# Performance work log

Hardware: AMD Instinct MI355X
Metric: run time of the kernel (lower is better)

## Reference

```python
import jax, jax.numpy as jnp
import numpy as np

B, S = 4, 2048
DM, H, DK, DV, DI = 512, 4, 128, 128, 1024
NT, NV = 64, 5000
PAD = 0


def layernorm(x, g, b, eps=1e-5):
    m = jnp.mean(x, axis=-1, keepdims=True)
    v = jnp.var(x, axis=-1, keepdims=True)
    return (x - m) * jax.lax.rsqrt(v + eps) * g + b


def setup_inputs() -> dict:
    key = jax.random.key(0)
    ks = jax.random.split(key, 20)
    event_type = jax.random.randint(ks[0], (B, S), 0, NT + 1)
    vertex = jax.random.randint(ks[1], (B, S), 0, NV + 1)
    vertex = jnp.where(event_type == PAD, 0, vertex)  # align padding
    event_time = jnp.sort(jax.random.uniform(ks[2], (B, S)) * 100.0, axis=1)
    non_pad_mask = (event_type != PAD).astype(jnp.float32)[..., None]  # [B,S,1]
    sc = 0.02
    event_emb = jax.random.normal(ks[3], (NT + 1, DM)) * sc
    event_emb = event_emb.at[PAD].set(0.0)
    vertex_emb = jax.random.normal(ks[4], (NV + 1, DM)) * sc
    vertex_emb = vertex_emb.at[PAD].set(0.0)
    A = jax.random.uniform(ks[5], (NV, NV))
    W = jax.random.uniform(ks[6], (NV, NV))
    Wq = jax.random.normal(ks[7], (DM, H * DK)) * sc
    Wk = jax.random.normal(ks[8], (DM, H * DK)) * sc
    Wv = jax.random.normal(ks[9], (DM, H * DV)) * sc
    Wo = jax.random.normal(ks[10], (H * DV, DM)) * sc
    bo = jnp.zeros((DM,))
    ln1_g, ln1_b = jnp.ones((DM,)), jnp.zeros((DM,))
    w1 = jax.random.normal(ks[11], (DM, DI)) * sc
    b1 = jnp.zeros((DI,))
    w2 = jax.random.normal(ks[12], (DI, DM)) * sc
    b2 = jnp.zeros((DM,))
    ln2_g, ln2_b = jnp.ones((DM,)), jnp.zeros((DM,))
    return dict(event_type=event_type, vertex=vertex, event_time=event_time,
                non_pad_mask=non_pad_mask, A=A, W=W, event_emb=event_emb,
                vertex_emb=vertex_emb, Wq=Wq, Wk=Wk, Wv=Wv, Wo=Wo, bo=bo,
                ln1_g=ln1_g, ln1_b=ln1_b, w1=w1, b1=b1, w2=w2, b2=b2,
                ln2_g=ln2_g, ln2_b=ln2_b)


def similarity(vertex, A, W):
    # vectorized form of the triple-loop pairwise gather: [B,1,S,S]
    idx = jnp.clip(vertex - 1, 0)                       # [B,S]
    vm = (vertex != 0)
    pair = vm[:, :, None] & vm[:, None, :]              # [B,S,S]
    sim = A[idx[:, :, None], idx[:, None, :]] * W[idx[:, :, None], idx[:, None, :]] * 10.0
    return (sim * pair.astype(A.dtype))[:, None]        # [B,1,S,S]


def temporal_enc(event_time, non_pad_mask, d_model):
    i = jnp.arange(d_model)
    pv = jnp.power(jnp.float32(10000.0), 2.0 * (i // 2).astype(jnp.float32) / d_model)
    r = event_time[:, :, None] / pv                     # [B,S,D]
    return jnp.where(i % 2 == 0, jnp.sin(r), jnp.cos(r)) * non_pad_mask


def reference(event_type, vertex, event_time, non_pad_mask, A, W, event_emb,
              vertex_emb, Wq, Wk, Wv, Wo, bo, ln1_g, ln1_b, w1, b1, w2, b2,
              ln2_g, ln2_b):
    b_, s_ = event_type.shape
    # masks: key-padding OR subsequent (causal)
    pad = (event_type == PAD)
    subseq = jnp.triu(jnp.ones((s_, s_), dtype=bool), 1)
    slf_attn_mask = pad[:, None, :] | subseq[None]      # [B,S,S]

    sim = similarity(vertex, A, W)                      # [B,1,S,S]
    tem = temporal_enc(event_time, non_pad_mask, DM)    # [B,S,D]
    ver = vertex_emb[vertex]                            # [B,S,D]
    enc = event_emb[event_type]                         # [B,S,D]

    # single encoder layer (n_layers=1), post-norm THP-style
    enc = enc + ver + tem
    res = enc
    q = (enc @ Wq).reshape(b_, s_, H, DK)
    k = (enc @ Wk).reshape(b_, s_, H, DK)
    v = (enc @ Wv).reshape(b_, s_, H, DV)
    scores = jnp.einsum('bihd,bjhd->bhij', q, k) / jnp.sqrt(jnp.float32(DK)) + sim
    scores = jnp.where(slf_attn_mask[:, None], jnp.float32(-1e9), scores)
    attn = jax.nn.softmax(scores, axis=-1)
    o = jnp.einsum('bhij,bjhd->bihd', attn, v).reshape(b_, s_, H * DV)
    o = o @ Wo + bo
    enc = layernorm(o + res, ln1_g, ln1_b) * non_pad_mask
    res = enc
    f = jax.nn.relu(enc @ w1 + b1) @ w2 + b2
    enc = layernorm(f + res, ln2_g, ln2_b) * non_pad_mask
    return enc, sim
```

## Files before the change

### kernel.cpp

```cpp
#include <hip/hip_runtime.h>
#include <hip/hip_bf16.h>

#define B_ 4
#define S_ 2048
#define DM_ 512
#define H_ 4
#define DK_ 128
#define DI_ 1024
#define NV_ 5000

typedef __attribute__((ext_vector_type(8))) short bf16x8;
typedef __attribute__((ext_vector_type(8))) unsigned short u16x8;
typedef __attribute__((ext_vector_type(4))) unsigned short u16x4;
typedef __attribute__((ext_vector_type(4))) float f32x4;

__device__ inline unsigned short f2bf(float x) {
  unsigned int u = __float_as_uint(x);
  unsigned int r = (u + 0x7fffu + ((u >> 16) & 1u)) >> 16;
  return (unsigned short)r;
}
__device__ inline float bf2f(unsigned short u) {
  return __uint_as_float(((unsigned int)u) << 16);
}
__device__ inline void gload16(const void* g, void* l) {
  __builtin_amdgcn_global_load_lds(
      (const __attribute__((address_space(1))) void*)g,
      (__attribute__((address_space(3))) void*)l, 16, 0, 0);
}

__global__ __launch_bounds__(256) void embed_kernel(
    const int* __restrict__ et, const int* __restrict__ vx,
    const float* __restrict__ tmv, const float* __restrict__ npm,
    const float* __restrict__ eemb, const float* __restrict__ vemb,
    float* __restrict__ enc0, unsigned short* __restrict__ enc0b) {
  int row = blockIdx.x;
  int t = et[row], v = vx[row];
  float time = tmv[row], mask = npm[row];
  int tid = threadIdx.x;
  #pragma unroll
  for (int k = 0; k < 2; ++k) {
    int dd = tid + k * 256;
    float pvinv = __expf((float)(dd & ~1) * -0.017988946039015984f);
    float r = time * pvinv;
    float tem = (((dd & 1) == 0) ? sinf(r) : cosf(r)) * mask;
    float val = eemb[(size_t)t * DM_ + dd] + vemb[(size_t)v * DM_ + dd] + tem;
    enc0[(size_t)row * DM_ + dd] = val;
    enc0b[(size_t)row * DM_ + dd] = f2bf(val);
  }
}

__global__ __launch_bounds__(256) void sim_kernel(
    const int* __restrict__ vx, const float* __restrict__ A,
    const float* __restrict__ W, float* __restrict__ sim) {
  __shared__ __attribute__((aligned(16))) float Ar[5120];
  __shared__ __attribute__((aligned(16))) float Wr[5120];
  int i = blockIdx.x;
  int b = blockIdx.y;
  int vi = vx[b * S_ + i];
  float* out = sim + ((size_t)(b * S_ + i)) * S_;
  int tid = threadIdx.x;
  if (vi == 0) {
    for (int j = tid * 4; j < S_; j += 1024)
      *(float4*)&out[j] = (float4){0.f, 0.f, 0.f, 0.f};
    return;
  }
  int w = tid >> 6, l = tid & 63;
  const char* Abase = (const char*)(A + (size_t)(vi - 1) * NV_);
  const char* Wbase = (const char*)(W + (size_t)(vi - 1) * NV_);
  #pragma unroll
  for (int it = 0; it < 5; ++it) {
    int seg = it * 4 + w;
    int chunk = seg * 64 + l;
    if (chunk < 1250) {
      gload16(Abase + (size_t)chunk * 16, (char*)Ar + seg * 1024);
      gload16(Wbase + (size_t)chunk * 16, (char*)Wr + seg * 1024);
    }
  }
  asm volatile("s_waitcnt vmcnt(0)" ::: "memory");
  __syncthreads();
  for (int j = tid * 4; j < S_; j += 1024) {
    int4 vj = *(const int4*)&vx[b * S_ + j];
    float4 o;
    o.x = vj.x ? Ar[vj.x - 1] * Wr[vj.x - 1] * 10.0f : 0.f;
    o.y = vj.y ? Ar[vj.y - 1] * Wr[vj.y - 1] * 10.0f : 0.f;
    o.z = vj.z ? Ar[vj.z - 1] * Wr[vj.z - 1] * 10.0f : 0.f;
    o.w = vj.w ? Ar[vj.w - 1] * Wr[vj.w - 1] * 10.0f : 0.f;
    *(float4*)&out[j] = o;
  }
}

__global__ __launch_bounds__(256) void wt_all_kernel(
    const float* __restrict__ Wq, const float* __restrict__ Wk,
    const float* __restrict__ Wv, const float* __restrict__ Wo,
    const float* __restrict__ w1, const float* __restrict__ w2,
    unsigned short* __restrict__ WqT, unsigned short* __restrict__ WkT,
    unsigned short* __restrict__ WvT, unsigned short* __restrict__ WoT,
    unsigned short* __restrict__ w1T, unsigned short* __restrict__ w2T) {
  __shared__ unsigned short T[32][40];
  int bid = blockIdx.x;
  const float* src; unsigned short* dst; int K, N, lid;
  if (bid < 256)       { src = Wq; dst = WqT; K = 512;  N = 512;  lid = bid; }
  else if (bid < 512)  { src = Wk; dst = WkT; K = 512;  N = 512;  lid = bid - 256; }
  else if (bid < 768)  { src = Wv; dst = WvT; K = 512;  N = 512;  lid = bid - 512; }
  else if (bid < 1024) { src = Wo; dst = WoT; K = 512;  N = 512;  lid = bid - 768; }
  else if (bid < 1536) { src = w1; dst = w1T; K = 512;  N = 1024; lid = bid - 1024; }
  else                 { src = w2; dst = w2T; K = 1024; N = 512;  lid = bid - 1536; }
  int nt = N / 32;
  int n0 = (lid % nt) * 32, k0 = (lid / nt) * 32;
  int r = threadIdx.x >> 3, c0 = (threadIdx.x & 7) * 4;
  float4 v = *(const float4*)&src[(size_t)(k0 + r) * N + n0 + c0];
  T[r][c0 + 0] = f2bf(v.x);
  T[r][c0 + 1] = f2bf(v.y);
  T[r][c0 + 2] = f2bf(v.z);
  T[r][c0 + 3] = f2bf(v.w);
  __syncthreads();
  u16x4 o;
  o[0] = T[c0 + 0][r]; o[1] = T[c0 + 1][r];
  o[2] = T[c0 + 2][r]; o[3] = T[c0 + 3][r];
  *(u16x4*)&dst[(size_t)(n0 + r) * K + k0 + c0] = o;
}

template <int OMODE, bool RELU, int MT = 128>
__global__ __launch_bounds__(256) void gemm_bf16_kernel(
    const unsigned short* __restrict__ A, const unsigned short* __restrict__ BT,
    const float* __restrict__ bias, void* __restrict__ C,
    int M, int N, int K) {
  __shared__ __attribute__((aligned(16))) unsigned short As[MT][72];
  __shared__ __attribute__((aligned(16))) unsigned short Bs[128][72];
  int tid = threadIdx.x;
  int w = tid >> 6, l = tid & 63;
  int l16 = l & 15, lh = l >> 4;
  const int NFR = (MT == 128) ? 4 : 2;
  int wr = (MT == 128) ? (w >> 1) : 0;
  int wc = (MT == 128) ? (w & 1) : w;
  int row0 = blockIdx.y * MT, col0 = blockIdx.x * 128;
  int ra = tid >> 1, ha = (tid & 1) * 32;
  f32x4 acc[4][4];
  #pragma unroll
  for (int m = 0; m < 4; ++m)
    #pragma unroll
    for (int n = 0; n < NFR; ++n) acc[m][n] = (f32x4){0.f, 0.f, 0.f, 0.f};

  for (int k0 = 0; k0 < K; k0 += 64) {
    __syncthreads();
    if (MT == 128) {
      const unsigned short* sa = &A[(size_t)(row0 + ra) * K + k0 + ha];
      uint4 a0 = *(const uint4*)(sa);
      uint4 a1 = *(const uint4*)(sa + 8);
      uint4 a2 = *(const uint4*)(sa + 16);
      uint4 a3 = *(const uint4*)(sa + 24);
      *(uint4*)&As[ra][ha + 0] = a0;
      *(uint4*)&As[ra][ha + 8] = a1;
      *(uint4*)&As[ra][ha + 16] = a2;
      *(uint4*)&As[ra][ha + 24] = a3;
    } else {
      int ra2 = tid >> 2, ha2 = (tid & 3) * 16;
      const unsigned short* sa = &A[(size_t)(row0 + ra2) * K + k0 + ha2];
      uint4 a0 = *(const uint4*)(sa);
      uint4 a1 = *(const uint4*)(sa + 8);
      *(uint4*)&As[ra2][ha2 + 0] = a0;
      *(uint4*)&As[ra2][ha2 + 8] = a1;
    }
    {
      const unsigned short* sb = &BT[(size_t)(col0 + ra) * K + k0 + ha];
      uint4 b0 = *(const uint4*)(sb);
      uint4 b1 = *(const uint4*)(sb + 8);
      uint4 b2 = *(const uint4*)(sb + 16);
      uint4 b3 = *(const uint4*)(sb + 24);
      *(uint4*)&Bs[ra][ha + 0] = b0;
      *(uint4*)&Bs[ra][ha + 8] = b1;
      *(uint4*)&Bs[ra][ha + 16] = b2;
      *(uint4*)&Bs[ra][ha + 24] = b3;
    }
    __syncthreads();
    #pragma unroll
    for (int kc = 0; kc < 2; ++kc) {
      bf16x8 af[4], bfr[4];
      #pragma unroll
      for (int m = 0; m < 4; ++m)
        af[m] = *(bf16x8*)&As[wr * 64 + m * 16 + l16][kc * 32 + lh * 8];
      #pragma unroll
      for (int n = 0; n < NFR; ++n)
        bfr[n] = *(bf16x8*)&Bs[wc * (16 * NFR) + n * 16 + l16][kc * 32 + lh * 8];
      #pragma unroll
      for (int m = 0; m < 4; ++m)
        #pragma unroll
        for (int n = 0; n < NFR; ++n)
          acc[m][n] = __builtin_amdgcn_mfma_f32_16x16x32_bf16(af[m], bfr[n], acc[m][n], 0, 0, 0);
    }
  }
  #pragma unroll
  for (int m = 0; m < 4; ++m) {
    #pragma unroll
    for (int r = 0; r < 4; ++r) {
      int row = row0 + wr * 64 + m * 16 + lh * 4 + r;
      #pragma unroll
      for (int n = 0; n < NFR; ++n) {
        int colg = col0 + wc * (16 * NFR) + n * 16 + l16;
        float v = acc[m][n][r];
        if (bias) v += bias[colg];
        if (RELU) v = fmaxf(v, 0.f);
        if (OMODE == 0) {
          ((float*)C)[(size_t)row * N + colg] = v;
        } else if (OMODE == 1) {
          ((unsigned short*)C)[(size_t)row * N + colg] = f2bf(v);
        } else {
          int which = colg >> 9;
          int cl = colg & 511;
          int b = row >> 11, s = row & 2047;
          int h = cl >> 7, d = cl & 127;
          unsigned short* base =
              (unsigned short*)C + (size_t)which * (4194304);
          if (which < 2)
            base[((size_t)((b * 4 + h) * 2048 + s)) * 128 + d] = f2bf(v);
          else
            base[((size_t)((b * 4 + h) * 128 + d)) * 2048 + s] = f2bf(v);
        }
      }
    }
  }
}

__global__ __launch_bounds__(256) void attn_mfma_kernel(
    const unsigned short* __restrict__ Qb, const unsigned short* __restrict__ Kb,
    const unsigned short* __restrict__ Vt, const float* __restrict__ sim,
    const float* __restrict__ npm, unsigned short* __restrict__ Op0,
    unsigned short* __restrict__ Op1, float2* __restrict__ ml0,
    float2* __restrict__ ml1) {
  __shared__ __attribute__((aligned(16))) char KsL[2][16384];
  __shared__ __attribute__((aligned(16))) char VtsL[2][16384];
  __shared__ __attribute__((aligned(16))) unsigned short Pl[4][16][72];
  int bid = blockIdx.x;
  int xcd = bid & 7;
  int j0 = bid >> 3;
  int bh = xcd * 2 + (j0 & 1);
  int jj = j0 >> 1;
  int pair = jj & 15;
  int half = jj >> 4;
  int b = bh >> 2;
  int tid = threadIdx.x;
  int w = tid >> 6, l = tid & 63;
  int l16 = l & 15, lh = l >> 4;
  unsigned short* Op = half ? Op1 : Op0;
  float2* ml = half ? ml1 : ml0;

  const char* KbB = (const char*)Kb + (size_t)bh * 2048 * 256;
  const char* VtB = (const char*)Vt + (size_t)bh * 128 * 4096;
  int krow[4], kcol[4], vrow4[4], vcol[4];
  #pragma unroll
  for (int j = 0; j < 4; ++j) {
    int i = w * 4 + j;
    krow[j] = i * 4 + (l >> 4);
    kcol[j] = ((l & 15) * 16) ^ ((krow[j] & 7) << 4);
    vrow4[j] = i * 8 + (l >> 3);
    vcol[j] = ((l & 7) * 16) ^ ((vrow4[j] & 7) << 4);
  }
  int xr = (l16 & 7) << 4;

  #pragma unroll 1
  for (int pj = 0; pj < 2; ++pj) {
    int qt = pj ? 31 - pair : pair;
    int nst = qt + 1;
    int c0 = (nst + 1) >> 1;
    int t0 = half ? c0 : 0;
    int cnt = half ? nst - c0 : c0;
    int q0 = qt * 64 + w * 16;
    int qg = q0 + l16;

    bf16x8 qf[4];
    const unsigned short* Qrow = Qb + ((size_t)(bh * 2048 + qg)) * 128;
    #pragma unroll
    for (int kq = 0; kq < 4; ++kq)
      qf[kq] = *(const bf16x8*)&Qrow[kq * 32 + lh * 8];

    float m_l = -INFINITY, l_l = 0.f;
    f32x4 o_acc[8];
    #pragma unroll
    for (int c = 0; c < 8; ++c) o_acc[c] = (f32x4){0.f, 0.f, 0.f, 0.f};

    const float* simrow = sim + ((size_t)(b * 2048) + qg) * 2048;
    const float* mrow = npm + b * 2048;

    if (cnt > 0) {
      #pragma unroll
      for (int j = 0; j < 4; ++j) {
        int i = w * 4 + j;
        gload16(KbB + (size_t)(t0 * 64 + krow[j]) * 256 + kcol[j],
                &KsL[0][i * 1024]);
        gload16(VtB + (size_t)vrow4[j] * 4096 + (size_t)(t0 * 64) * 2 + vcol[j],
                &VtsL[0][i * 1024]);
      }
      asm volatile("s_waitcnt vmcnt(0)" ::: "memory");
      __syncthreads();

      #pragma unroll 1
      for (int ti = 0; ti < cnt; ++ti) {
        int cur = ti & 1;
        int kv0 = (t0 + ti) * 64;
        if (ti + 1 < cnt) {
          int kvn = kv0 + 64;
          #pragma unroll
          for (int j = 0; j < 4; ++j) {
            int i = w * 4 + j;
            gload16(KbB + (size_t)(kvn + krow[j]) * 256 + kcol[j],
                    &KsL[cur ^ 1][i * 1024]);
            gload16(VtB + (size_t)vrow4[j] * 4096 + (size_t)kvn * 2 + vcol[j],
                    &VtsL[cur ^ 1][i * 1024]);
          }
        }
        const char* Kbase = KsL[cur];
        f32x4 sc[4];
        #pragma unroll
        for (int tt = 0; tt < 4; ++tt) {
          sc[tt] = (f32x4){0.f, 0.f, 0.f, 0.f};
          const char* Krow = Kbase + (tt * 16 + l16) * 256;
          #pragma unroll
          for (int kq = 0; kq < 4; ++kq) {
            bf16x8 kf = *(const bf16x8*)(Krow + ((kq * 64 + lh * 16) ^ xr));
            sc[tt] = __builtin_amdgcn_mfma_f32_16x16x32_bf16(kf, qf[kq], sc[tt], 0, 0, 0);
          }
        }
        float4 sim4[4], mk4[4];
        #pragma unroll
        for (int tt = 0; tt < 4; ++tt) {
          sim4[tt] = *(const float4*)&simrow[kv0 + tt * 16 + lh * 4];
          mk4[tt] = *(const float4*)&mrow[kv0 + tt * 16 + lh * 4];
        }
        float sv[4][4];
        #pragma unroll
        for (int tt = 0; tt < 4; ++tt) {
          #pragma unroll
          for (int r = 0; r < 4; ++r) {
            int kvg = kv0 + tt * 16 + lh * 4 + r;
            float mkr = r == 0 ? mk4[tt].x : r == 1 ? mk4[tt].y
                      : r == 2 ? mk4[tt].z : mk4[tt].w;
            float smr = r == 0 ? sim4[tt].x : r == 1 ? sim4[tt].y
                      : r == 2 ? sim4[tt].z : sim4[tt].w;
            bool valid = (kvg <= qg) && (mkr != 0.f);
            sv[tt][r] = valid ? sc[tt][r] * 0.08838834764831845f + smr : -1e9f;
          }
        }
        float mx = sv[0][0];
        #pragma unroll
        for (int tt = 0; tt < 4; ++tt)
          #pragma unroll
          for (int r = 0; r < 4; ++r) mx = fmaxf(mx, sv[tt][r]);
        mx = fmaxf(mx, __shfl_xor(mx, 16));
        mx = fmaxf(mx, __shfl_xor(mx, 32));
        float mn = fmaxf(m_l, mx);
        float alpha = __expf(m_l - mn);
        m_l = mn;
        float ts = 0.f;
        #pragma unroll
        for (int tt = 0; tt < 4; ++tt)
          #pragma unroll
          for (int r = 0; r < 4; ++r) {
            float ppv = __expf(sv[tt][r] - mn);
            sv[tt][r] = ppv;
            ts += ppv;
          }
        ts += __shfl_xor(ts, 16);
        ts += __shfl_xor(ts, 32);
        l_l = l_l * alpha + ts;
        #pragma unroll
        for (int tt = 0; tt < 4; ++tt) {
          u16x4 pw;
          pw[0] = f2bf(sv[tt][0]); pw[1] = f2bf(sv[tt][1]);
          pw[2] = f2bf(sv[tt][2]); pw[3] = f2bf(sv[tt][3]);
          *(u16x4*)&Pl[w][l16][tt * 16 + lh * 4] = pw;
        }
        float al[4];
        #pragma unroll
        for (int r = 0; r < 4; ++r) al[r] = __shfl(alpha, lh * 4 + r);
        #pragma unroll
        for (int c = 0; c < 8; ++c)
          #pragma unroll
          for (int r = 0; r < 4; ++r) o_acc[c][r] *= al[r];
        const char* Vbase = VtsL[cur];
        #pragma unroll
        for (int kf2 = 0; kf2 < 2; ++kf2) {
          bf16x8 pa = *(bf16x8*)&Pl[w][l16][kf2 * 32 + lh * 8];
          #pragma unroll
          for (int c = 0; c < 8; ++c) {
            bf16x8 vf = *(const bf16x8*)(Vbase + (c * 16 + l16) * 128 +
                                         ((kf2 * 64 + lh * 16) ^ xr));
            o_acc[c] = __builtin_amdgcn_mfma_f32_16x16x32_bf16(pa, vf, o_acc[c], 0, 0, 0);
          }
        }
        asm volatile("s_waitcnt vmcnt(0)" ::: "memory");
        __syncthreads();
      }
    }
    #pragma unroll
    for (int r = 0; r < 4; ++r) {
      int qgr = q0 + lh * 4 + r;
      unsigned short* op = Op + ((size_t)(bh * 2048 + qgr)) * 128;
      #pragma unroll
      for (int c = 0; c < 8; ++c) op[c * 16 + l16] = f2bf(o_acc[c][r]);
    }
    if (lh == 0) {
      float2 v; v.x = m_l; v.y = l_l;
      ml[bh * 2048 + q0 + l16] = v;
    }
    __syncthreads();
  }
}

__global__ __launch_bounds__(256) void attn_combine_kernel(
    const unsigned short* __restrict__ Op0, const unsigned short* __restrict__ Op1,
    const float2* __restrict__ ml0, const float2* __restrict__ ml1,
    unsigned short* __restrict__ Of) {
  int idx = blockIdx.x * 256 + threadIdx.x;
  int row = idx >> 4;
  int d0 = (idx & 15) * 8;
  float2 a = ml0[row], c2 = ml1[row];
  float m = fmaxf(a.x, c2.x);
  float e1 = __expf(a.x - m), e2 = __expf(c2.x - m);
  float inv = 1.f / (e1 * a.y + e2 * c2.y);
  u16x8 o1 = *(const u16x8*)&Op0[(size_t)row * 128 + d0];
  u16x8 o2 = *(const u16x8*)&Op1[(size_t)row * 128 + d0];
  int bh = row >> 11, q = row & 2047;
  int b = bh >> 2, h = bh & 3;
  unsigned short* dst = Of + ((size_t)(b * 2048 + q)) * 512 + h * 128 + d0;
  u16x8 o;
  #pragma unroll
  for (int j = 0; j < 8; ++j)
    o[j] = f2bf((bf2f(o1[j]) * e1 + bf2f(o2[j]) * e2) * inv);
  *(u16x8*)dst = o;
}

__global__ __launch_bounds__(256) void ln_kernel(
    const float* __restrict__ x, const float* __restrict__ res,
    const float* __restrict__ g, const float* __restrict__ bta,
    const float* __restrict__ npm, float* __restrict__ out,
    unsigned short* __restrict__ out16) {
  __shared__ float ssum[4], ssq[4];
  int row = blockIdx.x;
  int tid = threadIdx.x;
  size_t base = (size_t)row * DM_;
  float v0 = x[base + tid] + res[base + tid];
  float v1 = x[base + tid + 256] + res[base + tid + 256];
  float sum = v0 + v1, sq = v0 * v0 + v1 * v1;
  #pragma unroll
  for (int off = 32; off >= 1; off >>= 1) {
    sum += __shfl_down(sum, off);
    sq += __shfl_down(sq, off);
  }
  int wid = tid >> 6, lane = tid & 63;
  if (lane == 0) { ssum[wid] = sum; ssq[wid] = sq; }
  __syncthreads();
  sum = ssum[0] + ssum[1] + ssum[2] + ssum[3];
  sq = ssq[0] + ssq[1] + ssq[2] + ssq[3];
  float mean = sum * (1.f / DM_);
  float var = sq * (1.f / DM_) - mean * mean;
  float rs = rsqrtf(var + 1e-5f);
  float mask = npm[row];
  float o0 = ((v0 - mean) * rs * g[tid] + bta[tid]) * mask;
  float o1 = ((v1 - mean) * rs * g[tid + 256] + bta[tid + 256]) * mask;
  out[base + tid] = o0;
  out[base + tid + 256] = o1;
  if (out16) {
    out16[base + tid] = f2bf(o0);
    out16[base + tid + 256] = f2bf(o1);
  }
}

extern "C" void kernel_launch(void* const* d_in, const int* in_sizes, int n_in,
                              void* d_out, int out_size, void* d_ws,
                              size_t ws_size, hipStream_t stream) {
  const int* et = (const int*)d_in[0];
  const int* vx = (const int*)d_in[1];
  const float* tmv = (const float*)d_in[2];
  const float* npm = (const float*)d_in[3];
  const float* Amat = (const float*)d_in[4];
  const float* Wmat = (const float*)d_in[5];
  const float* eemb = (const float*)d_in[6];
  const float* vemb = (const float*)d_in[7];
  const float* Wq = (const float*)d_in[8];
  const float* Wk = (const float*)d_in[9];
  const float* Wv = (const float*)d_in[10];
  const float* Wo = (const float*)d_in[11];
  const float* bo = (const float*)d_in[12];
  const float* ln1g = (const float*)d_in[13];
  const float* ln1b = (const float*)d_in[14];
  const float* w1 = (const float*)d_in[15];
  const float* b1 = (const float*)d_in[16];
  const float* w2 = (const float*)d_in[17];
  const float* b2 = (const float*)d_in[18];
  const float* ln2g = (const float*)d_in[19];
  const float* ln2b = (const float*)d_in[20];

  float* out = (float*)d_out;
  float* enc_out = out;
  float* sim_out = out + (size_t)B_ * S_ * DM_;

  const size_t MB = 1ull << 20;
  char* wsb = (char*)d_ws;
  float* enc0 = (float*)(wsb + 0);
  unsigned short* enc0b = (unsigned short*)(wsb + 16 * MB);
  unsigned short* WqT = (unsigned short*)(wsb + 24 * MB);
  unsigned short* WkT = WqT + 512 * 512;
  unsigned short* WvT = WkT + 512 * 512;
  unsigned short* WoT = WvT + 512 * 512;
  unsigned short* w1T = WoT + 512 * 512;
  unsigned short* w2T = w1T + 1024 * 512;
  unsigned short* Qb16 = (unsigned short*)(wsb + 28 * MB);
  unsigned short* Kb16 = (unsigned short*)(wsb + 36 * MB);
  unsigned short* Vt16 = (unsigned short*)(wsb + 44 * MB);
  unsigned short* Op0 = (unsigned short*)(wsb + 52 * MB);
  unsigned short* Op1 = enc0b;
  float2* ml0 = (float2*)(wsb + 60 * MB);
  float2* ml1 = ml0 + 32768;
  unsigned short* Of16 = Qb16;
  float* OP = (float*)(wsb + 88 * MB);
  float* enc1 = OP;
  unsigned short* enc1b = enc0b;
  unsigned short* hid = Kb16;
  float* fbuf = (float*)(wsb + 52 * MB);

  int M = B_ * S_;

  embed_kernel<<<dim3(M), dim3(256), 0, stream>>>(et, vx, tmv, npm, eemb, vemb,
                                                  enc0, enc0b);
  sim_kernel<<<dim3(S_, B_), dim3(256), 0, stream>>>(vx, Amat, Wmat, sim_out);

  wt_all_kernel<<<dim3(2048), dim3(256), 0, stream>>>(
      Wq, Wk, Wv, Wo, w1, w2, WqT, WkT, WvT, WoT, w1T, w2T);

  gemm_bf16_kernel<5, false, 64><<<dim3(12, 128), dim3(256), 0, stream>>>(
      enc0b, WqT, nullptr, Qb16, M, 3 * DM_, DM_);

  attn_mfma_kernel<<<dim3(512), dim3(256), 0, stream>>>(
      Qb16, Kb16, Vt16, sim_out, npm, Op0, Op1, ml0, ml1);
  attn_combine_kernel<<<dim3(2048), dim3(256), 0, stream>>>(
      Op0, Op1, ml0, ml1, Of16);

  gemm_bf16_kernel<0, false, 64><<<dim3(4, 128), dim3(256), 0, stream>>>(
      Of16, WoT, bo, OP, M, DM_, DM_);
  ln_kernel<<<dim3(M), dim3(256), 0, stream>>>(OP, enc0, ln1g, ln1b, npm, enc1,
                                               enc1b);

  gemm_bf16_kernel<1, true, 64><<<dim3(8, 128), dim3(256), 0, stream>>>(
      enc1b, w1T, b1, hid, M, DI_, DM_);
  gemm_bf16_kernel<0, false, 64><<<dim3(4, 128), dim3(256), 0, stream>>>(
      hid, w2T, b2, fbuf, M, DM_, DI_);
  ln_kernel<<<dim3(M), dim3(256), 0, stream>>>(fbuf, enc1, ln2g, ln2b, npm,
                                               enc_out, nullptr);
}
```

Before: 272.6 us.

## Merge embed with weight transpose, and sim with QKV GEMM into combined launches

Combines the embedding kernel and the weight transpose/convert kernel into one launch, split by block index. It also combines the similarity-matrix kernel with the QKV projection GEMM into a single grid, so the memory-bound sim writes can overlap with the MFMA GEMM blocks. The aim is to cut launch count and fill idle compute units by co-scheduling independent work. The combined simqkv kernel uses a 40KB shared arena for both roles, which may limit occupancy for the GEMM part. The QKV GEMM is reimplemented inline without the templated kernel's structure.

```diff
diff --git a/kernel.cpp b/kernel.cpp
--- a/kernel.cpp
+++ b/kernel.cpp
@@ -28,96 +28,175 @@
       (__attribute__((address_space(3))) void*)l, 16, 0, 0);
 }
 
-__global__ __launch_bounds__(256) void embed_kernel(
+__global__ __launch_bounds__(256) void ew_kernel(
     const int* __restrict__ et, const int* __restrict__ vx,
     const float* __restrict__ tmv, const float* __restrict__ npm,
     const float* __restrict__ eemb, const float* __restrict__ vemb,
-    float* __restrict__ enc0, unsigned short* __restrict__ enc0b) {
-  int row = blockIdx.x;
-  int t = et[row], v = vx[row];
-  float time = tmv[row], mask = npm[row];
-  int tid = threadIdx.x;
-  #pragma unroll
-  for (int k = 0; k < 2; ++k) {
-    int dd = tid + k * 256;
-    float pvinv = __expf((float)(dd & ~1) * -0.017988946039015984f);
-    float r = time * pvinv;
-    float tem = (((dd & 1) == 0) ? sinf(r) : cosf(r)) * mask;
-    float val = eemb[(size_t)t * DM_ + dd] + vemb[(size_t)v * DM_ + dd] + tem;
-    enc0[(size_t)row * DM_ + dd] = val;
-    enc0b[(size_t)row * DM_ + dd] = f2bf(val);
-  }
-}
-
-__global__ __launch_bounds__(256) void sim_kernel(
-    const int* __restrict__ vx, const float* __restrict__ A,
-    const float* __restrict__ W, float* __restrict__ sim) {
-  __shared__ __attribute__((aligned(16))) float Ar[5120];
-  __shared__ __attribute__((aligned(16))) float Wr[5120];
-  int i = blockIdx.x;
-  int b = blockIdx.y;
-  int vi = vx[b * S_ + i];
-  float* out = sim + ((size_t)(b * S_ + i)) * S_;
-  int tid = threadIdx.x;
-  if (vi == 0) {
-    for (int j = tid * 4; j < S_; j += 1024)
-      *(float4*)&out[j] = (float4){0.f, 0.f, 0.f, 0.f};
-    return;
-  }
-  int w = tid >> 6, l = tid & 63;
-  const char* Abase = (const char*)(A + (size_t)(vi - 1) * NV_);
-  const char* Wbase = (const char*)(W + (size_t)(vi - 1) * NV_);
-  #pragma unroll
-  for (int it = 0; it < 5; ++it) {
-    int seg = it * 4 + w;
-    int chunk = seg * 64 + l;
-    if (chunk < 1250) {
-      gload16(Abase + (size_t)chunk * 16, (char*)Ar + seg * 1024);
-      gload16(Wbase + (size_t)chunk * 16, (char*)Wr + seg * 1024);
-    }
-  }
-  asm volatile("s_waitcnt vmcnt(0)" ::: "memory");
-  __syncthreads();
-  for (int j = tid * 4; j < S_; j += 1024) {
-    int4 vj = *(const int4*)&vx[b * S_ + j];
-    float4 o;
-    o.x = vj.x ? Ar[vj.x - 1] * Wr[vj.x - 1] * 10.0f : 0.f;
-    o.y = vj.y ? Ar[vj.y - 1] * Wr[vj.y - 1] * 10.0f : 0.f;
-    o.z = vj.z ? Ar[vj.z - 1] * Wr[vj.z - 1] * 10.0f : 0.f;
-    o.w = vj.w ? Ar[vj.w - 1] * Wr[vj.w - 1] * 10.0f : 0.f;
-    *(float4*)&out[j] = o;
-  }
-}
-
-__global__ __launch_bounds__(256) void wt_all_kernel(
     const float* __restrict__ Wq, const float* __restrict__ Wk,
     const float* __restrict__ Wv, const float* __restrict__ Wo,
     const float* __restrict__ w1, const float* __restrict__ w2,
+    float* __restrict__ enc0, unsigned short* __restrict__ enc0b,
     unsigned short* __restrict__ WqT, unsigned short* __restrict__ WkT,
     unsigned short* __restrict__ WvT, unsigned short* __restrict__ WoT,
     unsigned short* __restrict__ w1T, unsigned short* __restrict__ w2T) {
   __shared__ unsigned short T[32][40];
   int bid = blockIdx.x;
-  const float* src; unsigned short* dst; int K, N, lid;
-  if (bid < 256)       { src = Wq; dst = WqT; K = 512;  N = 512;  lid = bid; }
-  else if (bid < 512)  { src = Wk; dst = WkT; K = 512;  N = 512;  lid = bid - 256; }
-  else if (bid < 768)  { src = Wv; dst = WvT; K = 512;  N = 512;  lid = bid - 512; }
-  else if (bid < 1024) { src = Wo; dst = WoT; K = 512;  N = 512;  lid = bid - 768; }
-  else if (bid < 1536) { src = w1; dst = w1T; K = 512;  N = 1024; lid = bid - 1024; }
-  else                 { src = w2; dst = w2T; K = 1024; N = 512;  lid = bid - 1536; }
-  int nt = N / 32;
-  int n0 = (lid % nt) * 32, k0 = (lid / nt) * 32;
-  int r = threadIdx.x >> 3, c0 = (threadIdx.x & 7) * 4;
-  float4 v = *(const float4*)&src[(size_t)(k0 + r) * N + n0 + c0];
-  T[r][c0 + 0] = f2bf(v.x);
-  T[r][c0 + 1] = f2bf(v.y);
-  T[r][c0 + 2] = f2bf(v.z);
-  T[r][c0 + 3] = f2bf(v.w);
-  __syncthreads();
-  u16x4 o;
-  o[0] = T[c0 + 0][r]; o[1] = T[c0 + 1][r];
-  o[2] = T[c0 + 2][r]; o[3] = T[c0 + 3][r];
-  *(u16x4*)&dst[(size_t)(n0 + r) * K + k0 + c0] = o;
+  int tid = threadIdx.x;
+  if (bid < 8192) {
+    int row = bid;
+    int t = et[row], v = vx[row];
+    float time = tmv[row], mask = npm[row];
+    #pragma unroll
+    for (int k = 0; k < 2; ++k) {
+      int dd = tid + k * 256;
+      float pvinv = __expf((float)(dd & ~1) * -0.017988946039015984f);
+      float r = time * pvinv;
+      float tem = (((dd & 1) == 0) ? sinf(r) : cosf(r)) * mask;
+      float val = eemb[(size_t)t * DM_ + dd] + vemb[(size_t)v * DM_ + dd] + tem;
+      enc0[(size_t)row * DM_ + dd] = val;
+      enc0b[(size_t)row * DM_ + dd] = f2bf(val);
+    }
+  } else {
+    int wb = bid - 8192;
+    const float* src; unsigned short* dst; int K, N, lid;
+    if (wb < 256)       { src = Wq; dst = WqT; K = 512;  N = 512;  lid = wb; }
+    else if (wb < 512)  { src = Wk; dst = WkT; K = 512;  N = 512;  lid = wb - 256; }
+    else if (wb < 768)  { src = Wv; dst = WvT; K = 512;  N = 512;  lid = wb - 512; }
+    else if (wb < 1024) { src = Wo; dst = WoT; K = 512;  N = 512;  lid = wb - 768; }
+    else if (wb < 1536) { src = w1; dst = w1T; K = 512;  N = 1024; lid = wb - 1024; }
+    else                { src = w2; dst = w2T; K = 1024; N = 512;  lid = wb - 1536; }
+    int nt = N / 32;
+    int n0 = (lid % nt) * 32, k0 = (lid / nt) * 32;
+    int r = tid >> 3, c0 = (tid & 7) * 4;
+    float4 v = *(const float4*)&src[(size_t)(k0 + r) * N + n0 + c0];
+    T[r][c0 + 0] = f2bf(v.x);
+    T[r][c0 + 1] = f2bf(v.y);
+    T[r][c0 + 2] = f2bf(v.z);
+    T[r][c0 + 3] = f2bf(v.w);
+    __syncthreads();
+    u16x4 o;
+    o[0] = T[c0 + 0][r]; o[1] = T[c0 + 1][r];
+    o[2] = T[c0 + 2][r]; o[3] = T[c0 + 3][r];
+    *(u16x4*)&dst[(size_t)(n0 + r) * K + k0 + c0] = o;
+  }
+}
+
+__global__ __launch_bounds__(256) void simqkv_kernel(
+    const int* __restrict__ vx, const float* __restrict__ A,
+    const float* __restrict__ W, float* __restrict__ sim,
+    const unsigned short* __restrict__ enc0b, const unsigned short* __restrict__ BT,
+    unsigned short* __restrict__ QKV) {
+  __shared__ __attribute__((aligned(16))) char arena[40960];
+  int bid = blockIdx.x;
+  int tid = threadIdx.x;
+  if (bid < 8192) {
+    float* Ar = (float*)arena;
+    float* Wr = (float*)(arena + 20480);
+    int i = bid & 2047;
+    int b = bid >> 11;
+    int vi = vx[b * S_ + i];
+    float* out = sim + ((size_t)(b * S_ + i)) * S_;
+    if (vi == 0) {
+      for (int j = tid * 4; j < S_; j += 1024)
+        *(float4*)&out[j] = (float4){0.f, 0.f, 0.f, 0.f};
+      return;
+    }
+    int w = tid >> 6, l = tid & 63;
+    const char* Abase = (const char*)(A + (size_t)(vi - 1) * NV_);
+    const char* Wbase = (const char*)(W + (size_t)(vi - 1) * NV_);
+    #pragma unroll
+    for (int it = 0; it < 5; ++it) {
+      int seg = it * 4 + w;
+      int chunk = seg * 64 + l;
+      if (chunk < 1250) {
+        gload16(Abase + (size_t)chunk * 16, (char*)Ar + seg * 1024);
+        gload16(Wbase + (size_t)chunk * 16, (char*)Wr + seg * 1024);
+      }
+    }
+    asm volatile("s_waitcnt vmcnt(0)" ::: "memory");
+    __syncthreads();
+    for (int j = tid * 4; j < S_; j += 1024) {
+      int4 vj = *(const int4*)&vx[b * S_ + j];
+      float4 o;
+      o.x = vj.x ? Ar[vj.x - 1] * Wr[vj.x - 1] * 10.0f : 0.f;
+      o.y = vj.y ? Ar[vj.y - 1] * Wr[vj.y - 1] * 10.0f : 0.f;
+      o.z = vj.z ? Ar[vj.z - 1] * Wr[vj.z - 1] * 10.0f : 0.f;
+      o.w = vj.w ? Ar[vj.w - 1] * Wr[vj.w - 1] * 10.0f : 0.f;
+      *(float4*)&out[j] = o;
+    }
+  } else {
+    unsigned short* As = (unsigned short*)arena;
+    unsigned short* Bs = (unsigned short*)(arena + 9216);
+    int qb = bid - 8192;
+    int bx = qb % 12, by = qb / 12;
+    int w = tid >> 6, l = tid & 63;
+    int l16 = l & 15, lh = l >> 4;
+    int row0 = by * 64, col0 = bx * 128;
+    int ra = tid >> 1, ha = (tid & 1) * 32;
+    int ra2 = tid >> 2, ha2 = (tid & 3) * 16;
+    f32x4 acc[4][2];
+    #pragma unroll
+    for (int m = 0; m < 4; ++m)
+      #pragma unroll
+      for (int n = 0; n < 2; ++n) acc[m][n] = (f32x4){0.f, 0.f, 0.f, 0.f};
+
+    for (int k0 = 0; k0 < 512; k0 += 64) {
+      __syncthreads();
+      {
+        const unsigned short* sa = &enc0b[(size_t)(row0 + ra2) * 512 + k0 + ha2];
+        uint4 a0 = *(const uint4*)(sa);
+        uint4 a1 = *(const uint4*)(sa + 8);
+        *(uint4*)&As[ra2 * 72 + ha2 + 0] = a0;
+        *(uint4*)&As[ra2 * 72 + ha2 + 8] = a1;
+        const unsigned short* sb = &BT[(size_t)(col0 + ra) * 512 + k0 + ha];
+        uint4 b0 = *(const uint4*)(sb);
+        uint4 b1 = *(const uint4*)(sb + 8);
+        uint4 b2 = *(const uint4*)(sb + 16);
+        uint4 b3 = *(const uint4*)(sb + 24);
+        *(uint4*)&Bs[ra * 72 + ha + 0] = b0;
+        *(uint4*)&Bs[ra * 72 + ha + 8] = b1;
+        *(uint4*)&Bs[ra * 72 + ha + 16] = b2;
+        *(uint4*)&Bs[ra * 72 + ha + 24] = b3;
+      }
+      __syncthreads();
+      #pragma unroll
+      for (int kc = 0; kc < 2; ++kc) {
+        bf16x8 af[4], bfr[2];
+        #pragma unroll
+        for (int m = 0; m < 4; ++m)
+          af[m] = *(bf16x8*)&As[(m * 16 + l16) * 72 + kc * 32 + lh * 8];
+        #pragma unroll
+        for (int n = 0; n < 2; ++n)
+          bfr[n] = *(bf16x8*)&Bs[(w * 32 + n * 16 + l16) * 72 + kc * 32 + lh * 8];
+        #pragma unroll
+        for (int m = 0; m < 4; ++m)
+          #pragma unroll
+          for (int n = 0; n < 2; ++n)
+            acc[m][n] = __builtin_amdgcn_mfma_f32_16x16x32_bf16(af[m], bfr[n], acc[m][n], 0, 0, 0);
+      }
+    }
+    #pragma unroll
+    for (int m = 0; m < 4; ++m) {
+      #pragma unroll
+      for (int r = 0; r < 4; ++r) {
+        int row = row0 + m * 16 + lh * 4 + r;
+        #pragma unroll
+        for (int n = 0; n < 2; ++n) {
+          int colg = col0 + w * 32 + n * 16 + l16;
+          float v = acc[m][n][r];
+          int which = colg >> 9;
+          int cl = colg & 511;
+          int b = row >> 11, s = row & 2047;
+          int h = cl >> 7, d = cl & 127;
+          unsigned short* base = QKV + (size_t)which * 4194304;
+          if (which < 2)
+            base[((size_t)((b * 4 + h) * 2048 + s)) * 128 + d] = f2bf(v);
+          else
+            base[((size_t)((b * 4 + h) * 128 + d)) * 2048 + s] = f2bf(v);
+        }
+      }
+    }
+  }
 }
 
 template <int OMODE, bool RELU, int MT = 128>
@@ -202,19 +281,8 @@
         if (RELU) v = fmaxf(v, 0.f);
         if (OMODE == 0) {
           ((float*)C)[(size_t)row * N + colg] = v;
-        } else if (OMODE == 1) {
+        } else {
           ((unsigned short*)C)[(size_t)row * N + colg] = f2bf(v);
-        } else {
-          int which = colg >> 9;
-          int cl = colg & 511;
-          int b = row >> 11, s = row & 2047;
-          int h = cl >> 7, d = cl & 127;
-          unsigned short* base =
-              (unsigned short*)C + (size_t)which * (4194304);
-          if (which < 2)
-            base[((size_t)((b * 4 + h) * 2048 + s)) * 128 + d] = f2bf(v);
-          else
-            base[((size_t)((b * 4 + h) * 128 + d)) * 2048 + s] = f2bf(v);
         }
       }
     }
@@ -520,15 +588,12 @@
 
   int M = B_ * S_;
 
-  embed_kernel<<<dim3(M), dim3(256), 0, stream>>>(et, vx, tmv, npm, eemb, vemb,
-                                                  enc0, enc0b);
-  sim_kernel<<<dim3(S_, B_), dim3(256), 0, stream>>>(vx, Amat, Wmat, sim_out);
-
-  wt_all_kernel<<<dim3(2048), dim3(256), 0, stream>>>(
-      Wq, Wk, Wv, Wo, w1, w2, WqT, WkT, WvT, WoT, w1T, w2T);
-
-  gemm_bf16_kernel<5, false, 64><<<dim3(12, 128), dim3(256), 0, stream>>>(
-      enc0b, WqT, nullptr, Qb16, M, 3 * DM_, DM_);
+  ew_kernel<<<dim3(10240), dim3(256), 0, stream>>>(
+      et, vx, tmv, npm, eemb, vemb, Wq, Wk, Wv, Wo, w1, w2,
+      enc0, enc0b, WqT, WkT, WvT, WoT, w1T, w2T);
+
+  simqkv_kernel<<<dim3(9728), dim3(256), 0, stream>>>(
+      vx, Amat, Wmat, sim_out, enc0b, WqT, Qb16);
 
   attn_mfma_kernel<<<dim3(512), dim3(256), 0, stream>>>(
       Qb16, Kb16, Vt16, sim_out, npm, Op0, Op1, ml0, ml1);
```

Result: faster. 263.6 us (-3.3%).
